# Optimization experiments

Hardware: AMD Instinct MI355X
Metric: run time of the kernel (lower is better)

## Reference

```python
import jax, jax.numpy as jnp
import numpy as np

D_MODEL = 64
N_HEADS = 4
D_K = 16
D_FF = 512
N_LAYERS = 6
SRC_V = 83
DEG_V = 21
DIST_V = 200
B, L = 256, 128


def _positional_encoding(length, d_model):
    pos = np.arange(length, dtype=np.float32)[:, None]
    div = np.exp(np.arange(0, d_model, 2, dtype=np.float32) * (-np.log(10000.0) / d_model))
    pe = np.zeros((length, d_model), dtype=np.float32)
    pe[:, 0::2] = np.sin(pos * div)
    pe[:, 1::2] = np.cos(pos * div)
    return jnp.asarray(pe)


def _layernorm(x, eps=1e-5):
    mu = jnp.mean(x, axis=-1, keepdims=True)
    var = jnp.mean((x - mu) ** 2, axis=-1, keepdims=True)
    return (x - mu) / jnp.sqrt(var + eps)


def setup_inputs() -> dict:
    key = jax.random.key(0)
    ks = jax.random.split(key, 12)
    s = 0.02
    enc_inputs = jax.random.randint(ks[0], (B, L), 0, SRC_V)
    degree_s = jax.random.randint(ks[1], (B, L), 0, DEG_V)
    MD = jax.random.randint(ks[2], (B, L, L), 0, DIST_V)
    src_emb = (jax.random.normal(ks[3], (SRC_V, D_MODEL)) * s).at[0].set(0.0)   # padding_idx=0
    deg_emb = (jax.random.normal(ks[4], (DEG_V, D_MODEL)) * s).at[20].set(0.0)  # padding_idx=20
    md_emb = (jax.random.normal(ks[5], (DIST_V, N_HEADS)) * s).at[0].set(0.0)   # padding_idx=0
    Wq = jax.random.normal(ks[6], (N_LAYERS, D_MODEL, N_HEADS * D_K)) * s
    Wk = jax.random.normal(ks[7], (N_LAYERS, D_MODEL, N_HEADS * D_K)) * s
    Wv = jax.random.normal(ks[8], (N_LAYERS, D_MODEL, N_HEADS * D_K)) * s
    Wo = jax.random.normal(ks[9], (N_LAYERS, N_HEADS * D_K, D_MODEL)) * s
    W1 = jax.random.normal(ks[10], (N_LAYERS, D_MODEL, D_FF)) * s
    W2 = jax.random.normal(ks[11], (N_LAYERS, D_FF, D_MODEL)) * s
    return dict(enc_inputs=enc_inputs, degree_s=degree_s, MD=MD,
                src_emb=src_emb, deg_emb=deg_emb, md_emb=md_emb,
                Wq=Wq, Wk=Wk, Wv=Wv, Wo=Wo, W1=W1, W2=W2)


def reference(enc_inputs, degree_s, MD, src_emb, deg_emb, md_emb, Wq, Wk, Wv, Wo, W1, W2):
    b, l = enc_inputs.shape
    x = src_emb[enc_inputs] + deg_emb[degree_s] + _positional_encoding(l, D_MODEL)[None]
    # pad mask: key token == 0 -> masked; broadcast [B,1,1,L] over heads & queries
    pad_mask = (enc_inputs == 0)[:, None, None, :]
    # distance bias: [B,L,L,H] -> [B,H,L,L]
    bias = jnp.transpose(md_emb[MD], (0, 3, 1, 2))
    scale = 1.0 / np.sqrt(D_K).astype(np.float32)
    for i in range(N_LAYERS):
        q = (x @ Wq[i]).reshape(b, l, N_HEADS, D_K).transpose(0, 2, 1, 3)
        k = (x @ Wk[i]).reshape(b, l, N_HEADS, D_K).transpose(0, 2, 1, 3)
        v = (x @ Wv[i]).reshape(b, l, N_HEADS, D_K).transpose(0, 2, 1, 3)
        scores = jnp.einsum('bhqd,bhkd->bhqk', q, k) * scale + bias
        scores = jnp.where(pad_mask, -1e9, scores)
        attn = jax.nn.softmax(scores, axis=-1)
        ctx = jnp.einsum('bhqk,bhkd->bhqd', attn, v).transpose(0, 2, 1, 3).reshape(b, l, N_HEADS * D_K)
        x = _layernorm(ctx @ Wo[i] + x)
        x = _layernorm(jax.nn.relu(x @ W1[i]) @ W2[i] + x)
    return x
```

## Files before the change

### kernel.cpp

```cpp
#include <hip/hip_runtime.h>
#include <hip/hip_bf16.h>
#include <stdint.h>

#define DI __device__ __forceinline__

namespace {

constexpr int BB  = 256;
constexpr int LL  = 128;
constexpr int DM  = 64;
constexpr int DFF = 512;
constexpr int NL  = 6;
constexpr int TT  = BB * LL;

typedef __attribute__((ext_vector_type(8))) short bf16x8;
typedef __attribute__((ext_vector_type(4))) float f32x4;

DI float bf2f(uint16_t u) { union { uint32_t i; float f; } w; w.i = (uint32_t)u << 16; return w.f; }
DI uint16_t f2bf(float f) {
  union { float f; uint32_t i; } w; w.f = f;
  uint32_t r = (w.i + 0x7fffu + ((w.i >> 16) & 1u)) >> 16;
  return (uint16_t)r;
}
DI uint32_t pack2(float a, float b) { return (uint32_t)f2bf(a) | ((uint32_t)f2bf(b) << 16); }

DI bf16x8 fragld(const uint16_t* __restrict__ base, int ld, int lane) {
  return *(const bf16x8*)(base + (size_t)(lane & 15) * ld + (lane >> 4) * 8);
}
DI f32x4 MFMA(bf16x8 a, bf16x8 b, f32x4 c) {
  return __builtin_amdgcn_mfma_f32_16x16x32_bf16(a, b, c, 0, 0, 0);
}

__global__ void __launch_bounds__(256) k_embed(const int* __restrict__ enc, const int* __restrict__ deg,
    const float* __restrict__ semb, const float* __restrict__ demb,
    float* __restrict__ x, uint16_t* __restrict__ xb) {
  int idx = blockIdx.x * 256 + threadIdx.x;
  int t = idx >> 6, d = idx & 63;
  int l = t & (LL - 1);
  float e = (float)(d & ~1) * -0.14391156831212787f;
  float ang = (float)l * __expf(e);
  float pe = (d & 1) ? __cosf(ang) : __sinf(ang);
  float v = semb[enc[t] * DM + d] + demb[deg[t] * DM + d] + pe;
  x[idx] = v;
  xb[idx] = f2bf(v);
}

__global__ void __launch_bounds__(256) k_trans(const float* __restrict__ w, uint16_t* __restrict__ wt,
    int K, int O, int dstStride, int colOff) {
  int idx = blockIdx.x * 256 + threadIdx.x;
  int KO = K * O;
  int mat = idx / KO;
  int rem = idx - mat * KO;
  int c = rem / K;
  int k = rem - c * K;
  wt[(size_t)mat * dstStride + (size_t)(colOff + c) * K + k] = f2bf(w[((size_t)mat * K + k) * O + c]);
}

__global__ void __launch_bounds__(256) k_bias2(const int* __restrict__ MD, const float* __restrict__ memb,
    const int* __restrict__ enc, uint16_t* __restrict__ biasT) {
  int o = blockIdx.x * 256 + threadIdx.x;
  int b  = o >> 14;
  int r  = (o >> 7) & (LL - 1);
  int kk = o & (LL - 1);
  bool mask = (enc[b * LL + kk] == 0);
  int md = MD[o];
  float4 m = *(const float4*)(memb + md * 4);
  float mv[4] = {m.x, m.y, m.z, m.w};
#pragma unroll
  for (int h = 0; h < 4; ++h) {
    uint16_t v = mask ? (uint16_t)0xce6eu : f2bf(mv[h]);
    biasT[(((size_t)(b * 4 + h) * LL) + r) * LL + kk] = v;
  }
}

DI void ln_write(float (&v)[4][4], float (&xfh)[4][4], uint16_t* __restrict__ xls,
                 int r0, int g, int c) {
  float sum[4], sq[4];
#pragma unroll
  for (int j = 0; j < 4; ++j) sum[j] = (v[j][0] + v[j][1]) + (v[j][2] + v[j][3]);
#pragma unroll
  for (int off = 1; off < 16; off <<= 1)
#pragma unroll
    for (int j = 0; j < 4; ++j) sum[j] += __shfl_xor(sum[j], off, 64);
#pragma unroll
  for (int j = 0; j < 4; ++j) {
    float mu = sum[j] * 0.015625f;
#pragma unroll
    for (int ct = 0; ct < 4; ++ct) v[j][ct] -= mu;
    sq[j] = (v[j][0] * v[j][0] + v[j][1] * v[j][1]) + (v[j][2] * v[j][2] + v[j][3] * v[j][3]);
  }
#pragma unroll
  for (int off = 1; off < 16; off <<= 1)
#pragma unroll
    for (int j = 0; j < 4; ++j) sq[j] += __shfl_xor(sq[j], off, 64);
#pragma unroll
  for (int j = 0; j < 4; ++j) {
    float rstd = rsqrtf(sq[j] * 0.015625f + 1e-5f);
#pragma unroll
    for (int ct = 0; ct < 4; ++ct) {
      float r = v[j][ct] * rstd;
      xfh[ct][j] = r;
      xls[(r0 + g * 4 + j) * 72 + ct * 16 + c] = f2bf(r);
    }
  }
}

constexpr int LDS_TOTAL = 138240;

template<int RT>
DI void attn_rt(bf16x8 (&cur)[4], bf16x8 (&nxt)[4],
                const uint16_t* __restrict__ bb, int hrow0,
                char* ptlb, uint16_t* qsc, const bf16x8 (&kf)[8],
                const uint16_t* vtlh, const uint2 (&qreg)[4], uint2 (&creg)[4],
                int lane, int g, int c) {
  int rl = lane >> 2, seg = lane & 3;
  int swz = (rl & 7) << 4;
  *(bf16x8*)(ptlb + rl * 256 + ((seg * 64 +  0) ^ swz)) = cur[0];
  *(bf16x8*)(ptlb + rl * 256 + ((seg * 64 + 16) ^ swz)) = cur[1];
  *(bf16x8*)(ptlb + rl * 256 + ((seg * 64 + 32) ^ swz)) = cur[2];
  *(bf16x8*)(ptlb + rl * 256 + ((seg * 64 + 48) ^ swz)) = cur[3];
  if (RT < 3) {
    const uint16_t* gs = bb + (size_t)(hrow0 + (RT + 1) * 16 + rl) * LL + seg * 32;
    nxt[0] = *(const bf16x8*)(gs);
    nxt[1] = *(const bf16x8*)(gs + 8);
    nxt[2] = *(const bf16x8*)(gs + 16);
    nxt[3] = *(const bf16x8*)(gs + 24);
  }
  qsc[(g * 4 + 0) * 40 + c] = (uint16_t)(qreg[RT].x & 0xffff);
  qsc[(g * 4 + 1) * 40 + c] = (uint16_t)(qreg[RT].x >> 16);
  qsc[(g * 4 + 2) * 40 + c] = (uint16_t)(qreg[RT].y & 0xffff);
  qsc[(g * 4 + 3) * 40 + c] = (uint16_t)(qreg[RT].y >> 16);
  bf16x8 qf = fragld(qsc, 40, lane);
  f32x4 s[8];
#pragma unroll
  for (int ct = 0; ct < 8; ++ct) s[ct] = MFMA(qf, kf[ct], (f32x4){0.f, 0.f, 0.f, 0.f});
  float rs[4] = {0.f, 0.f, 0.f, 0.f};
#pragma unroll
  for (int ct = 0; ct < 8; ++ct) {
    int kk = ct * 16 + c;
#pragma unroll
    for (int j = 0; j < 4; ++j) {
      int row = g * 4 + j;
      char* addr = ptlb + row * 256 + ((kk * 2) ^ ((row & 7) << 4));
      float bias = bf2f(*(uint16_t*)addr);
      float p = __expf(fmaf(s[ct][j], 0.25f, bias));
      rs[j] += p;
      *(uint16_t*)addr = f2bf(p);
    }
  }
#pragma unroll
  for (int off = 1; off < 16; off <<= 1)
#pragma unroll
    for (int j = 0; j < 4; ++j) rs[j] += __shfl_xor(rs[j], off, 64);
  bf16x8 vf[4];
#pragma unroll
  for (int kc = 0; kc < 4; ++kc) vf[kc] = fragld(vtlh + kc * 32, 136, lane);
  f32x4 o = {0.f, 0.f, 0.f, 0.f};
#pragma unroll
  for (int kc = 0; kc < 4; ++kc) {
    bf16x8 af = *(const bf16x8*)(ptlb + c * 256 + ((kc * 64 + g * 16) ^ ((c & 7) << 4)));
    o = MFMA(af, vf[kc], o);
  }
  creg[RT].x = pack2(o[0] / rs[0], o[1] / rs[1]);
  creg[RT].y = pack2(o[2] / rs[2], o[3] / rs[3]);
}

__global__ void __launch_bounds__(512, 1) k_mega(
    const float* __restrict__ x0, const uint16_t* __restrict__ xb0,
    const uint16_t* __restrict__ biasT,
    const uint16_t* __restrict__ wtqkv, const uint16_t* __restrict__ wto,
    const uint16_t* __restrict__ wt1, const uint16_t* __restrict__ wt2,
    float* __restrict__ out) {
  __shared__ __align__(16) char LDSB[LDS_TOTAL];
  int tid = threadIdx.x;
  int w8 = tid >> 6, lane = tid & 63;
  int g = lane >> 4, c = lane & 15;
  int h = w8 & 3, half = w8 >> 2;
  int b = blockIdx.x;

  uint16_t* xls  = (uint16_t*)(LDSB);
  char*     klsA = LDSB + 18432;
  uint16_t* klsh = (uint16_t*)(LDSB + 18432 + h * 10240);
  uint16_t* vtlh = (uint16_t*)(LDSB + 59392 + h * 4352);
  uint16_t* qsc  = (uint16_t*)(LDSB + 76800 + w8 * 1280);
  char*     ptlb = LDSB + 87040 + w8 * 4096;
  uint16_t* ctxl = (uint16_t*)(LDSB + 119808);
  uint16_t* hidl = (uint16_t*)(LDSB + 18432 + w8 * 8448);

  int r0 = w8 * 16;
  int hrow0 = half * 64;

  float xf[4][4];
  const float* xrow = x0 + ((size_t)b * LL + r0) * DM;
#pragma unroll
  for (int ct = 0; ct < 4; ++ct)
#pragma unroll
    for (int j = 0; j < 4; ++j)
      xf[ct][j] = xrow[(g * 4 + j) * DM + ct * 16 + c];
  {
    const uint16_t* xbrow = xb0 + (size_t)b * LL * DM;
#pragma unroll
    for (int m = 0; m < 2; ++m) {
      int u = tid * 2 + m;
      int r = u >> 3, col = (u & 7) * 8;
      *(bf16x8*)(xls + r * 72 + col) = *(const bf16x8*)(xbrow + r * DM + col);
    }
  }
  const uint16_t* bb = biasT + ((size_t)b * 4 + h) * (LL * LL);
  __syncthreads();

  for (int li = 0; li < NL; ++li) {
#pragma unroll
    for (int m = 0; m < 2; ++m) {
      int idx = tid * 2 + m;
      int head = idx >> 8, r = (idx >> 1) & 127, s2 = idx & 1;
      *(uint4*)(klsA + head * 10240 + r * 80 + 32 + s2 * 16) = uint4{0, 0, 0, 0};
    }
    if (lane < 32) {
      int r = lane >> 1, s2 = lane & 1;
      *(uint4*)((char*)qsc + r * 80 + 32 + s2 * 16) = uint4{0, 0, 0, 0};
    }

    const uint16_t* Wl = wtqkv + (size_t)li * 192 * 64;
    bf16x8 bq0 = fragld(Wl + (h * 16) * 64, 64, lane);
    bf16x8 bq1 = fragld(Wl + (h * 16) * 64 + 32, 64, lane);
    bf16x8 bk0 = fragld(Wl + (64 + h * 16) * 64, 64, lane);
    bf16x8 bk1 = fragld(Wl + (64 + h * 16) * 64 + 32, 64, lane);
    bf16x8 bv0 = fragld(Wl + (128 + h * 16) * 64, 64, lane);
    bf16x8 bv1 = fragld(Wl + (128 + h * 16) * 64 + 32, 64, lane);
    uint2 qreg[4];
#pragma unroll
    for (int rt = 0; rt < 4; ++rt) {
      int rr = hrow0 + rt * 16;
      bf16x8 a0 = fragld(xls + rr * 72, 72, lane);
      bf16x8 a1 = fragld(xls + rr * 72 + 32, 72, lane);
      f32x4 aq = {0,0,0,0}, ak = {0,0,0,0}, av = {0,0,0,0};
      aq = MFMA(a0, bq0, aq); aq = MFMA(a1, bq1, aq);
      ak = MFMA(a0, bk0, ak); ak = MFMA(a1, bk1, ak);
      av = MFMA(a0, bv0, av); av = MFMA(a1, bv1, av);
#pragma unroll
      for (int j = 0; j < 4; ++j)
        klsh[(rr + g * 4 + j) * 40 + c] = f2bf(ak[j]);
      uint2 pk; pk.x = pack2(av[0], av[1]); pk.y = pack2(av[2], av[3]);
      *(uint2*)(vtlh + c * 136 + rr + g * 4) = pk;
      qreg[rt].x = pack2(aq[0], aq[1]); qreg[rt].y = pack2(aq[2], aq[3]);
    }
    bf16x8 bregA[4], bregB[4];
    {
      int rl = lane >> 2, seg = lane & 3;
      const uint16_t* gs = bb + (size_t)(hrow0 + rl) * LL + seg * 32;
      bregA[0] = *(const bf16x8*)(gs);
      bregA[1] = *(const bf16x8*)(gs + 8);
      bregA[2] = *(const bf16x8*)(gs + 16);
      bregA[3] = *(const bf16x8*)(gs + 24);
    }
    __syncthreads();

    bf16x8 kf[8];
#pragma unroll
    for (int ct = 0; ct < 8; ++ct) kf[ct] = fragld(klsh + ct * 16 * 40, 40, lane);
    uint2 creg[4];
    attn_rt<0>(bregA, bregB, bb, hrow0, ptlb, qsc, kf, vtlh, qreg, creg, lane, g, c);
    attn_rt<1>(bregB, bregA, bb, hrow0, ptlb, qsc, kf, vtlh, qreg, creg, lane, g, c);
    attn_rt<2>(bregA, bregB, bb, hrow0, ptlb, qsc, kf, vtlh, qreg, creg, lane, g, c);
    attn_rt<3>(bregB, bregA, bb, hrow0, ptlb, qsc, kf, vtlh, qreg, creg, lane, g, c);

#pragma unroll
    for (int rt = 0; rt < 4; ++rt) {
      int rr = hrow0 + rt * 16;
      ctxl[(rr + g * 4 + 0) * 72 + h * 16 + c] = (uint16_t)(creg[rt].x & 0xffff);
      ctxl[(rr + g * 4 + 1) * 72 + h * 16 + c] = (uint16_t)(creg[rt].x >> 16);
      ctxl[(rr + g * 4 + 2) * 72 + h * 16 + c] = (uint16_t)(creg[rt].y & 0xffff);
      ctxl[(rr + g * 4 + 3) * 72 + h * 16 + c] = (uint16_t)(creg[rt].y >> 16);
    }
    __syncthreads();

    {
      const uint16_t* Wol = wto + (size_t)li * 64 * 64;
      bf16x8 a0 = fragld(ctxl + r0 * 72, 72, lane);
      bf16x8 a1 = fragld(ctxl + r0 * 72 + 32, 72, lane);
      float v[4][4];
#pragma unroll
      for (int ct = 0; ct < 4; ++ct) {
        f32x4 acc = {0,0,0,0};
        acc = MFMA(a0, fragld(Wol + ct * 16 * 64, 64, lane), acc);
        acc = MFMA(a1, fragld(Wol + ct * 16 * 64 + 32, 64, lane), acc);
#pragma unroll
        for (int j = 0; j < 4; ++j) v[j][ct] = acc[j] + xf[ct][j];
      }
      ln_write(v, xf, xls, r0, g, c);
    }

    {
      const uint16_t* W1l = wt1 + (size_t)li * 512 * 64;
      const uint16_t* W2l = wt2 + (size_t)li * 64 * 512;
      bf16x8 a0 = fragld(xls + r0 * 72, 72, lane);
      bf16x8 a1 = fragld(xls + r0 * 72 + 32, 72, lane);
      f32x4 acc2[4] = {{0,0,0,0},{0,0,0,0},{0,0,0,0},{0,0,0,0}};
#pragma unroll
      for (int fh = 0; fh < 2; ++fh) {
#pragma unroll 4
        for (int ct2 = 0; ct2 < 16; ++ct2) {
          int ctg = fh * 16 + ct2;
          f32x4 acc = {0,0,0,0};
          acc = MFMA(a0, fragld(W1l + ctg * 16 * 64, 64, lane), acc);
          acc = MFMA(a1, fragld(W1l + ctg * 16 * 64 + 32, 64, lane), acc);
#pragma unroll
          for (int j = 0; j < 4; ++j)
            hidl[(g * 4 + j) * 264 + ct2 * 16 + c] = f2bf(fmaxf(acc[j], 0.f));
        }
#pragma unroll 4
        for (int kc2 = 0; kc2 < 8; ++kc2) {
          bf16x8 a = fragld(hidl + kc2 * 32, 264, lane);
          int kg = fh * 256 + kc2 * 32;
#pragma unroll
          for (int ct = 0; ct < 4; ++ct)
            acc2[ct] = MFMA(a, fragld(W2l + ct * 16 * 512 + kg, 512, lane), acc2[ct]);
        }
      }
      float v[4][4];
#pragma unroll
      for (int ct = 0; ct < 4; ++ct)
#pragma unroll
        for (int j = 0; j < 4; ++j) v[j][ct] = acc2[ct][j] + xf[ct][j];
      ln_write(v, xf, xls, r0, g, c);
    }
    __syncthreads();
  }

  float* orow = out + ((size_t)b * LL + r0) * DM;
#pragma unroll
  for (int ct = 0; ct < 4; ++ct)
#pragma unroll
    for (int j = 0; j < 4; ++j)
      orow[(g * 4 + j) * DM + ct * 16 + c] = xf[ct][j];
}

}

extern "C" void kernel_launch(void* const* d_in, const int* in_sizes, int n_in,
                              void* d_out, int out_size, void* d_ws, size_t ws_size,
                              hipStream_t stream) {
  const int* enc = (const int*)d_in[0];
  const int* deg = (const int*)d_in[1];
  const int* MD  = (const int*)d_in[2];
  const float* semb = (const float*)d_in[3];
  const float* demb = (const float*)d_in[4];
  const float* memb = (const float*)d_in[5];
  const float* Wq = (const float*)d_in[6];
  const float* Wk = (const float*)d_in[7];
  const float* Wv = (const float*)d_in[8];
  const float* Wo = (const float*)d_in[9];
  const float* W1 = (const float*)d_in[10];
  const float* W2 = (const float*)d_in[11];

  char* p = (char*)d_ws;
  float*    x    = (float*)p;     p += (size_t)TT * DM * 4;
  uint16_t* xb   = (uint16_t*)p;  p += (size_t)TT * DM * 2;
  uint16_t* biasT = (uint16_t*)p; p += (size_t)BB * 4 * LL * LL * 2;
  uint16_t* wtqkv = (uint16_t*)p; p += (size_t)NL * 192 * 64 * 2;
  uint16_t* wto   = (uint16_t*)p; p += (size_t)NL * 64 * 64 * 2;
  uint16_t* wt1   = (uint16_t*)p; p += (size_t)NL * 512 * 64 * 2;
  uint16_t* wt2   = (uint16_t*)p; p += (size_t)NL * 64 * 512 * 2;
  (void)ws_size; (void)in_sizes; (void)n_in; (void)out_size;

  k_embed<<<TT * DM / 256, 256, 0, stream>>>(enc, deg, semb, demb, x, xb);
  k_trans<<<NL * 64 * 64 / 256, 256, 0, stream>>>(Wq, wtqkv, 64, 64, 192 * 64, 0);
  k_trans<<<NL * 64 * 64 / 256, 256, 0, stream>>>(Wk, wtqkv, 64, 64, 192 * 64, 64);
  k_trans<<<NL * 64 * 64 / 256, 256, 0, stream>>>(Wv, wtqkv, 64, 64, 192 * 64, 128);
  k_trans<<<NL * 64 * 64 / 256, 256, 0, stream>>>(Wo, wto, 64, 64, 64 * 64, 0);
  k_trans<<<NL * 64 * 512 / 256, 256, 0, stream>>>(W1, wt1, 64, 512, 512 * 64, 0);
  k_trans<<<NL * 512 * 64 / 256, 256, 0, stream>>>(W2, wt2, 512, 64, 64 * 512, 0);
  k_bias2<<<BB * LL * LL / 256, 256, 0, stream>>>(MD, memb, enc, biasT);

  k_mega<<<BB, 512, 0, stream>>>(x, xb, biasT, wtqkv, wto, wt1, wt2, (float*)d_out);
}
```

Measured before the change: 303.5 us.

## Process attention row tiles in pairs and repack LDS strides

Attention now handles two 16-row query tiles per call with two P buffers. This interleaves independent MFMA, exp and shuffle chains so more instruction-level parallelism hides latency, and bias prefetch now covers two tiles at a time. LDS strides for K, ctx, Q scratch and the FFN hidden buffer are shrunk. K and Q padding zeroing moves out of the layer loop into the prologue, and the FFN is split into four 128-wide chunks that are fully unrolled. The cost is higher register pressure from doubled live state, plus possible bank conflicts from the new strides.

```diff
diff --git a/kernel.cpp b/kernel.cpp
--- a/kernel.cpp
+++ b/kernel.cpp
@@ -105,64 +105,94 @@
   }
 }
 
-constexpr int LDS_TOTAL = 138240;
-
-template<int RT>
-DI void attn_rt(bf16x8 (&cur)[4], bf16x8 (&nxt)[4],
-                const uint16_t* __restrict__ bb, int hrow0,
-                char* ptlb, uint16_t* qsc, const bf16x8 (&kf)[8],
-                const uint16_t* vtlh, const uint2 (&qreg)[4], uint2 (&creg)[4],
-                int lane, int g, int c) {
+constexpr int OFF_KLS = 18432;
+constexpr int OFF_VTL = 39168;
+constexpr int OFF_HID = 18432;
+constexpr int OFF_CTX = 56576;
+constexpr int OFF_QSC = 73984;
+constexpr int OFF_PTL = 92416;
+constexpr int LDS_TOTAL = 157952;
+
+DI void attn_pair(bf16x8 (&bA)[4], bf16x8 (&bB)[4], bool prefetch,
+                  const uint16_t* __restrict__ bb, int nrow0,
+                  char* ptl0, char* ptl1, uint16_t* qscw,
+                  const bf16x8 (&kf)[8], const uint16_t* vtlh,
+                  uint2 q0, uint2 q1, uint2& cr0, uint2& cr1,
+                  int lane, int g, int c) {
   int rl = lane >> 2, seg = lane & 3;
   int swz = (rl & 7) << 4;
-  *(bf16x8*)(ptlb + rl * 256 + ((seg * 64 +  0) ^ swz)) = cur[0];
-  *(bf16x8*)(ptlb + rl * 256 + ((seg * 64 + 16) ^ swz)) = cur[1];
-  *(bf16x8*)(ptlb + rl * 256 + ((seg * 64 + 32) ^ swz)) = cur[2];
-  *(bf16x8*)(ptlb + rl * 256 + ((seg * 64 + 48) ^ swz)) = cur[3];
-  if (RT < 3) {
-    const uint16_t* gs = bb + (size_t)(hrow0 + (RT + 1) * 16 + rl) * LL + seg * 32;
-    nxt[0] = *(const bf16x8*)(gs);
-    nxt[1] = *(const bf16x8*)(gs + 8);
-    nxt[2] = *(const bf16x8*)(gs + 16);
-    nxt[3] = *(const bf16x8*)(gs + 24);
-  }
-  qsc[(g * 4 + 0) * 40 + c] = (uint16_t)(qreg[RT].x & 0xffff);
-  qsc[(g * 4 + 1) * 40 + c] = (uint16_t)(qreg[RT].x >> 16);
-  qsc[(g * 4 + 2) * 40 + c] = (uint16_t)(qreg[RT].y & 0xffff);
-  qsc[(g * 4 + 3) * 40 + c] = (uint16_t)(qreg[RT].y >> 16);
-  bf16x8 qf = fragld(qsc, 40, lane);
-  f32x4 s[8];
-#pragma unroll
-  for (int ct = 0; ct < 8; ++ct) s[ct] = MFMA(qf, kf[ct], (f32x4){0.f, 0.f, 0.f, 0.f});
-  float rs[4] = {0.f, 0.f, 0.f, 0.f};
+#pragma unroll
+  for (int m = 0; m < 4; ++m) {
+    *(bf16x8*)(ptl0 + rl * 256 + ((seg * 64 + m * 16) ^ swz)) = bA[m];
+    *(bf16x8*)(ptl1 + rl * 256 + ((seg * 64 + m * 16) ^ swz)) = bB[m];
+  }
+  if (prefetch) {
+    const uint16_t* gs0 = bb + (size_t)(nrow0 + rl) * LL + seg * 32;
+    const uint16_t* gs1 = gs0 + 16 * LL;
+#pragma unroll
+    for (int m = 0; m < 4; ++m) bA[m] = *(const bf16x8*)(gs0 + m * 8);
+#pragma unroll
+    for (int m = 0; m < 4; ++m) bB[m] = *(const bf16x8*)(gs1 + m * 8);
+  }
+  uint16_t* qs0 = qscw;
+  uint16_t* qs1 = qscw + 16 * 36;
+  qs0[(g * 4 + 0) * 36 + c] = (uint16_t)(q0.x & 0xffff);
+  qs0[(g * 4 + 1) * 36 + c] = (uint16_t)(q0.x >> 16);
+  qs0[(g * 4 + 2) * 36 + c] = (uint16_t)(q0.y & 0xffff);
+  qs0[(g * 4 + 3) * 36 + c] = (uint16_t)(q0.y >> 16);
+  qs1[(g * 4 + 0) * 36 + c] = (uint16_t)(q1.x & 0xffff);
+  qs1[(g * 4 + 1) * 36 + c] = (uint16_t)(q1.x >> 16);
+  qs1[(g * 4 + 2) * 36 + c] = (uint16_t)(q1.y & 0xffff);
+  qs1[(g * 4 + 3) * 36 + c] = (uint16_t)(q1.y >> 16);
+  bf16x8 qf0 = fragld(qs0, 36, lane);
+  bf16x8 qf1 = fragld(qs1, 36, lane);
+  f32x4 s0[8], s1[8];
+#pragma unroll
+  for (int ct = 0; ct < 8; ++ct) {
+    s0[ct] = MFMA(qf0, kf[ct], (f32x4){0.f, 0.f, 0.f, 0.f});
+    s1[ct] = MFMA(qf1, kf[ct], (f32x4){0.f, 0.f, 0.f, 0.f});
+  }
+  float rs0[4] = {0.f, 0.f, 0.f, 0.f}, rs1[4] = {0.f, 0.f, 0.f, 0.f};
 #pragma unroll
   for (int ct = 0; ct < 8; ++ct) {
     int kk = ct * 16 + c;
 #pragma unroll
     for (int j = 0; j < 4; ++j) {
       int row = g * 4 + j;
-      char* addr = ptlb + row * 256 + ((kk * 2) ^ ((row & 7) << 4));
-      float bias = bf2f(*(uint16_t*)addr);
-      float p = __expf(fmaf(s[ct][j], 0.25f, bias));
-      rs[j] += p;
-      *(uint16_t*)addr = f2bf(p);
+      int off = row * 256 + ((kk * 2) ^ ((row & 7) << 4));
+      char* a0 = ptl0 + off;
+      char* a1 = ptl1 + off;
+      float b0 = bf2f(*(uint16_t*)a0);
+      float b1 = bf2f(*(uint16_t*)a1);
+      float p0 = __expf(fmaf(s0[ct][j], 0.25f, b0));
+      float p1 = __expf(fmaf(s1[ct][j], 0.25f, b1));
+      rs0[j] += p0;
+      rs1[j] += p1;
+      *(uint16_t*)a0 = f2bf(p0);
+      *(uint16_t*)a1 = f2bf(p1);
     }
   }
 #pragma unroll
   for (int off = 1; off < 16; off <<= 1)
 #pragma unroll
-    for (int j = 0; j < 4; ++j) rs[j] += __shfl_xor(rs[j], off, 64);
+    for (int j = 0; j < 4; ++j) {
+      rs0[j] += __shfl_xor(rs0[j], off, 64);
+      rs1[j] += __shfl_xor(rs1[j], off, 64);
+    }
   bf16x8 vf[4];
 #pragma unroll
   for (int kc = 0; kc < 4; ++kc) vf[kc] = fragld(vtlh + kc * 32, 136, lane);
-  f32x4 o = {0.f, 0.f, 0.f, 0.f};
+  f32x4 o0 = {0.f, 0.f, 0.f, 0.f}, o1 = {0.f, 0.f, 0.f, 0.f};
 #pragma unroll
   for (int kc = 0; kc < 4; ++kc) {
-    bf16x8 af = *(const bf16x8*)(ptlb + c * 256 + ((kc * 64 + g * 16) ^ ((c & 7) << 4)));
-    o = MFMA(af, vf[kc], o);
-  }
-  creg[RT].x = pack2(o[0] / rs[0], o[1] / rs[1]);
-  creg[RT].y = pack2(o[2] / rs[2], o[3] / rs[3]);
+    int off = c * 256 + ((kc * 64 + g * 16) ^ ((c & 7) << 4));
+    o0 = MFMA(*(const bf16x8*)(ptl0 + off), vf[kc], o0);
+    o1 = MFMA(*(const bf16x8*)(ptl1 + off), vf[kc], o1);
+  }
+  cr0.x = pack2(o0[0] / rs0[0], o0[1] / rs0[1]);
+  cr0.y = pack2(o0[2] / rs0[2], o0[3] / rs0[3]);
+  cr1.x = pack2(o1[0] / rs1[0], o1[1] / rs1[1]);
+  cr1.y = pack2(o1[2] / rs1[2], o1[3] / rs1[3]);
 }
 
 __global__ void __launch_bounds__(512, 1) k_mega(
@@ -179,13 +209,13 @@
   int b = blockIdx.x;
 
   uint16_t* xls  = (uint16_t*)(LDSB);
-  char*     klsA = LDSB + 18432;
-  uint16_t* klsh = (uint16_t*)(LDSB + 18432 + h * 10240);
-  uint16_t* vtlh = (uint16_t*)(LDSB + 59392 + h * 4352);
-  uint16_t* qsc  = (uint16_t*)(LDSB + 76800 + w8 * 1280);
-  char*     ptlb = LDSB + 87040 + w8 * 4096;
-  uint16_t* ctxl = (uint16_t*)(LDSB + 119808);
-  uint16_t* hidl = (uint16_t*)(LDSB + 18432 + w8 * 8448);
+  uint16_t* klsh = (uint16_t*)(LDSB + OFF_KLS + h * 5184);
+  uint16_t* vtlh = (uint16_t*)(LDSB + OFF_VTL + h * 4352);
+  uint16_t* hidl = (uint16_t*)(LDSB + OFF_HID + w8 * 4480);
+  uint16_t* ctxl = (uint16_t*)(LDSB + OFF_CTX);
+  uint16_t* qscw = (uint16_t*)(LDSB + OFF_QSC + w8 * 2304);
+  char*     ptl0 = LDSB + OFF_PTL + w8 * 8192;
+  char*     ptl1 = ptl0 + 4096;
 
   int r0 = w8 * 16;
   int hrow0 = half * 64;
@@ -205,22 +235,15 @@
       int r = u >> 3, col = (u & 7) * 8;
       *(bf16x8*)(xls + r * 72 + col) = *(const bf16x8*)(xbrow + r * DM + col);
     }
+#pragma unroll
+    for (int m = 0; m < 18; ++m) qscw[lane + m * 64] = 0;
+    for (int o = tid * 16; o < 20736; o += 512 * 16)
+      *(uint4*)(LDSB + OFF_KLS + o) = uint4{0, 0, 0, 0};
   }
   const uint16_t* bb = biasT + ((size_t)b * 4 + h) * (LL * LL);
   __syncthreads();
 
   for (int li = 0; li < NL; ++li) {
-#pragma unroll
-    for (int m = 0; m < 2; ++m) {
-      int idx = tid * 2 + m;
-      int head = idx >> 8, r = (idx >> 1) & 127, s2 = idx & 1;
-      *(uint4*)(klsA + head * 10240 + r * 80 + 32 + s2 * 16) = uint4{0, 0, 0, 0};
-    }
-    if (lane < 32) {
-      int r = lane >> 1, s2 = lane & 1;
-      *(uint4*)((char*)qsc + r * 80 + 32 + s2 * 16) = uint4{0, 0, 0, 0};
-    }
-
     const uint16_t* Wl = wtqkv + (size_t)li * 192 * 64;
     bf16x8 bq0 = fragld(Wl + (h * 16) * 64, 64, lane);
     bf16x8 bq1 = fragld(Wl + (h * 16) * 64 + 32, 64, lane);
@@ -240,7 +263,7 @@
       av = MFMA(a0, bv0, av); av = MFMA(a1, bv1, av);
 #pragma unroll
       for (int j = 0; j < 4; ++j)
-        klsh[(rr + g * 4 + j) * 40 + c] = f2bf(ak[j]);
+        klsh[(rr + g * 4 + j) * 20 + c] = f2bf(ak[j]);
       uint2 pk; pk.x = pack2(av[0], av[1]); pk.y = pack2(av[2], av[3]);
       *(uint2*)(vtlh + c * 136 + rr + g * 4) = pk;
       qreg[rt].x = pack2(aq[0], aq[1]); qreg[rt].y = pack2(aq[2], aq[3]);
@@ -248,37 +271,38 @@
     bf16x8 bregA[4], bregB[4];
     {
       int rl = lane >> 2, seg = lane & 3;
-      const uint16_t* gs = bb + (size_t)(hrow0 + rl) * LL + seg * 32;
-      bregA[0] = *(const bf16x8*)(gs);
-      bregA[1] = *(const bf16x8*)(gs + 8);
-      bregA[2] = *(const bf16x8*)(gs + 16);
-      bregA[3] = *(const bf16x8*)(gs + 24);
+      const uint16_t* gs0 = bb + (size_t)(hrow0 + rl) * LL + seg * 32;
+      const uint16_t* gs1 = gs0 + 16 * LL;
+#pragma unroll
+      for (int m = 0; m < 4; ++m) bregA[m] = *(const bf16x8*)(gs0 + m * 8);
+#pragma unroll
+      for (int m = 0; m < 4; ++m) bregB[m] = *(const bf16x8*)(gs1 + m * 8);
     }
     __syncthreads();
 
     bf16x8 kf[8];
 #pragma unroll
-    for (int ct = 0; ct < 8; ++ct) kf[ct] = fragld(klsh + ct * 16 * 40, 40, lane);
+    for (int ct = 0; ct < 8; ++ct) kf[ct] = fragld(klsh + ct * 16 * 20, 20, lane);
     uint2 creg[4];
-    attn_rt<0>(bregA, bregB, bb, hrow0, ptlb, qsc, kf, vtlh, qreg, creg, lane, g, c);
-    attn_rt<1>(bregB, bregA, bb, hrow0, ptlb, qsc, kf, vtlh, qreg, creg, lane, g, c);
-    attn_rt<2>(bregA, bregB, bb, hrow0, ptlb, qsc, kf, vtlh, qreg, creg, lane, g, c);
-    attn_rt<3>(bregB, bregA, bb, hrow0, ptlb, qsc, kf, vtlh, qreg, creg, lane, g, c);
+    attn_pair(bregA, bregB, true,  bb, hrow0 + 32, ptl0, ptl1, qscw, kf, vtlh,
+              qreg[0], qreg[1], creg[0], creg[1], lane, g, c);
+    attn_pair(bregA, bregB, false, bb, 0,          ptl0, ptl1, qscw, kf, vtlh,
+              qreg[2], qreg[3], creg[2], creg[3], lane, g, c);
 
 #pragma unroll
     for (int rt = 0; rt < 4; ++rt) {
       int rr = hrow0 + rt * 16;
-      ctxl[(rr + g * 4 + 0) * 72 + h * 16 + c] = (uint16_t)(creg[rt].x & 0xffff);
-      ctxl[(rr + g * 4 + 1) * 72 + h * 16 + c] = (uint16_t)(creg[rt].x >> 16);
-      ctxl[(rr + g * 4 + 2) * 72 + h * 16 + c] = (uint16_t)(creg[rt].y & 0xffff);
-      ctxl[(rr + g * 4 + 3) * 72 + h * 16 + c] = (uint16_t)(creg[rt].y >> 16);
+      ctxl[(rr + g * 4 + 0) * 68 + h * 16 + c] = (uint16_t)(creg[rt].x & 0xffff);
+      ctxl[(rr + g * 4 + 1) * 68 + h * 16 + c] = (uint16_t)(creg[rt].x >> 16);
+      ctxl[(rr + g * 4 + 2) * 68 + h * 16 + c] = (uint16_t)(creg[rt].y & 0xffff);
+      ctxl[(rr + g * 4 + 3) * 68 + h * 16 + c] = (uint16_t)(creg[rt].y >> 16);
     }
     __syncthreads();
 
     {
       const uint16_t* Wol = wto + (size_t)li * 64 * 64;
-      bf16x8 a0 = fragld(ctxl + r0 * 72, 72, lane);
-      bf16x8 a1 = fragld(ctxl + r0 * 72 + 32, 72, lane);
+      bf16x8 a0 = fragld(ctxl + r0 * 68, 68, lane);
+      bf16x8 a1 = fragld(ctxl + r0 * 68 + 32, 68, lane);
       float v[4][4];
 #pragma unroll
       for (int ct = 0; ct < 4; ++ct) {
@@ -298,21 +322,21 @@
       bf16x8 a1 = fragld(xls + r0 * 72 + 32, 72, lane);
       f32x4 acc2[4] = {{0,0,0,0},{0,0,0,0},{0,0,0,0},{0,0,0,0}};
 #pragma unroll
-      for (int fh = 0; fh < 2; ++fh) {
-#pragma unroll 4
-        for (int ct2 = 0; ct2 < 16; ++ct2) {
-          int ctg = fh * 16 + ct2;
+      for (int fh = 0; fh < 4; ++fh) {
+#pragma unroll
+        for (int ct2 = 0; ct2 < 8; ++ct2) {
+          int ctg = fh * 8 + ct2;
           f32x4 acc = {0,0,0,0};
           acc = MFMA(a0, fragld(W1l + ctg * 16 * 64, 64, lane), acc);
           acc = MFMA(a1, fragld(W1l + ctg * 16 * 64 + 32, 64, lane), acc);
 #pragma unroll
           for (int j = 0; j < 4; ++j)
-            hidl[(g * 4 + j) * 264 + ct2 * 16 + c] = f2bf(fmaxf(acc[j], 0.f));
+            hidl[(g * 4 + j) * 140 + ct2 * 16 + c] = f2bf(fmaxf(acc[j], 0.f));
         }
-#pragma unroll 4
-        for (int kc2 = 0; kc2 < 8; ++kc2) {
-          bf16x8 a = fragld(hidl + kc2 * 32, 264, lane);
-          int kg = fh * 256 + kc2 * 32;
+#pragma unroll
+        for (int kc2 = 0; kc2 < 4; ++kc2) {
+          bf16x8 a = fragld(hidl + kc2 * 32, 140, lane);
+          int kg = fh * 128 + kc2 * 32;
 #pragma unroll
           for (int ct = 0; ct < 4; ++ct)
             acc2[ct] = MFMA(a, fragld(W2l + ct * 16 * 512 + kg, 512, lane), acc2[ct]);
```

New measurement: 327.7 us. 8.0% more time.
